# Performance work log

Measured on AMD Instinct MI355X. Metric: run time of the kernel, lower is better.

The kernel has to match this reference:

```python
import jax, jax.numpy as jnp
import numpy as np

N_NODES = 100000
N_EDGES = 1600000
D_IN = 128
D_OUT = 128


def setup_inputs() -> dict:
    key = jax.random.key(0)
    kx, ke, kw = jax.random.split(key, 3)
    x = jax.random.normal(kx, (N_NODES, D_IN), dtype=jnp.float32)
    edge_index = jax.random.randint(ke, (2, N_EDGES), 0, N_NODES, dtype=jnp.int32)
    W = jax.random.normal(kw, (D_IN, D_OUT), dtype=jnp.float32) / np.sqrt(D_IN)
    b = jnp.zeros((D_OUT,), dtype=jnp.float32)
    return {"x": x, "edge_index": edge_index, "W": W, "b": b}


def reference(x, edge_index, W, b):
    # PyG GCNConv: x' = D^{-1/2} (A + I) D^{-1/2} (x @ W) + b, then ReLU.
    n = x.shape[0]
    xw = x @ W  # linear transform first (as in GCNConv)
    # add self-loops
    loops = jnp.arange(n, dtype=edge_index.dtype)
    row = jnp.concatenate([edge_index[0], loops])  # source nodes
    col = jnp.concatenate([edge_index[1], loops])  # destination nodes
    # symmetric degree normalization (degree counted on destination, PyG-style)
    deg = jax.ops.segment_sum(jnp.ones_like(col, dtype=xw.dtype), col, num_segments=n)
    dinv = jnp.where(deg > 0, jax.lax.rsqrt(deg), 0.0)
    norm = dinv[row] * dinv[col]  # [E+N]
    # gather -> scale -> scatter-add
    msg = xw[row] * norm[:, None]  # [E+N, D_OUT]
    agg = jax.ops.segment_sum(msg, col, num_segments=n)  # [N, D_OUT]
    return jax.nn.relu(agg + b)
```

## Files before the change

kernel.cpp:

```cpp
#include <hip/hip_runtime.h>

#define DCH 128
#define T_PART 4096
#define B_MAX 512
#define CAPC 6144

typedef short bf16x8 __attribute__((ext_vector_type(8)));
typedef float f32x4 __attribute__((ext_vector_type(4)));

__device__ inline unsigned short f2bf(float f) {
    unsigned int u = __float_as_uint(f);
    unsigned int r = (u + 0x7fffu + ((u >> 16) & 1u)) >> 16;
    return (unsigned short)r;
}

__device__ inline void gload_lds16(const void* g, void* l) {
    __builtin_amdgcn_global_load_lds(
        (const __attribute__((address_space(1))) void*)g,
        (__attribute__((address_space(3))) void*)l, 16, 0, 0);
}

__global__ __launch_bounds__(256) void k_init(const float* __restrict__ W,
                                              unsigned short* __restrict__ Wf,
                                              int* __restrict__ gcount, int B) {
    int idx = blockIdx.x * 256 + threadIdx.x;
    if (idx < B) gcount[idx] = 0;
    int frag = blockIdx.x * 4 + (threadIdx.x >> 6);
    if (frag < 32) {
        int lane = threadIdx.x & 63;
        int nt = frag >> 2, ks = frag & 3;
        int nn = nt * 16 + (lane & 15);
        int k0 = ks * 32 + ((lane >> 4) * 8);
        unsigned short tmp[8];
#pragma unroll
        for (int j = 0; j < 8; ++j) tmp[j] = f2bf(W[(size_t)(k0 + j) * DCH + nn]);
        *(uint4*)&Wf[((size_t)frag * 64 + lane) * 8] = *(const uint4*)tmp;
    }
}

__global__ __launch_bounds__(512) void k_part(const int* __restrict__ row,
                                              const int* __restrict__ col,
                                              unsigned int* __restrict__ coarse,
                                              int* __restrict__ gcount,
                                              int E, int B) {
    __shared__ int hist[B_MAX];
    __shared__ int basex[B_MAX];
    __shared__ int curx[B_MAX];
    __shared__ int gb[B_MAX];
    __shared__ int wsum[8];
    __shared__ unsigned int spack[T_PART];
    __shared__ unsigned short sbuck[T_PART];

    int tid = threadIdx.x;
    int wv = tid >> 6, lane = tid & 63;
    int base_e = blockIdx.x * T_PART;
    int tileCnt = min(T_PART, E - base_e);

    hist[tid] = 0;
    __syncthreads();

    int er[8], ec[8];
#pragma unroll
    for (int i = 0; i < 8; ++i) {
        int e = base_e + tid + i * 512;
        if (e < E) {
            er[i] = row[e];
            ec[i] = col[e];
            atomicAdd(&hist[ec[i] >> 8], 1);
        } else {
            er[i] = -1;
            ec[i] = 0;
        }
    }
    __syncthreads();

    int v = hist[tid];
    int x = v;
#pragma unroll
    for (int o = 1; o < 64; o <<= 1) {
        int t = __shfl_up(x, o, 64);
        if (lane >= o) x += t;
    }
    if (lane == 63) wsum[wv] = x;
    __syncthreads();
    int add = 0;
    for (int w = 0; w < wv; ++w) add += wsum[w];
    int excl = x - v + add;
    basex[tid] = excl;
    curx[tid] = excl;
    if (tid < B) gb[tid] = (v > 0) ? atomicAdd(&gcount[tid], v) : 0;
    else gb[tid] = 0;
    __syncthreads();

#pragma unroll
    for (int i = 0; i < 8; ++i) {
        if (er[i] >= 0) {
            int b = ec[i] >> 8;
            int slot = atomicAdd(&curx[b], 1);
            spack[slot] = ((unsigned int)er[i] << 8) | (unsigned int)(ec[i] & 255);
            sbuck[slot] = (unsigned short)b;
        }
    }
    __syncthreads();

    for (int s = tid; s < tileCnt; s += 512) {
        int b = sbuck[s];
        int dst = gb[b] + (s - basex[b]);
        if (dst < CAPC) coarse[(size_t)b * CAPC + dst] = spack[s];
    }
}

__global__ __launch_bounds__(512) void k_csr(const unsigned int* __restrict__ coarse,
                                             const int* __restrict__ gcount,
                                             int* __restrict__ srow,
                                             int* __restrict__ off,
                                             int* __restrict__ cnt,
                                             int n, int B) {
    __shared__ unsigned int ent[CAPC];
    __shared__ int h[256], cur[256];
    __shared__ int red1[8], red2[4];
    __shared__ int bbase_s;

    int b = blockIdx.x;
    int tid = threadIdx.x;
    int wv = tid >> 6, lane = tid & 63;

    int part = 0;
    for (int i = tid; i < b; i += 512) part += gcount[i];
#pragma unroll
    for (int o = 1; o < 64; o <<= 1) part += __shfl_xor(part, o, 64);
    if (lane == 0) red1[wv] = part;
    if (tid < 256) h[tid] = 0;
    __syncthreads();
    if (tid == 0) {
        int s = 0;
        for (int w = 0; w < 8; ++w) s += red1[w];
        bbase_s = s;
    }
    int cntb = min(gcount[b], CAPC);
    for (int s = tid; s < cntb; s += 512) ent[s] = coarse[(size_t)b * CAPC + s];
    __syncthreads();

    for (int s = tid; s < cntb; s += 512) atomicAdd(&h[ent[s] & 255], 1);
    __syncthreads();

    int x = 0, v = 0;
    if (tid < 256) {
        v = h[tid];
        x = v;
#pragma unroll
        for (int o = 1; o < 64; o <<= 1) {
            int t = __shfl_up(x, o, 64);
            if (lane >= o) x += t;
        }
        if (lane == 63) red2[wv] = x;
    }
    __syncthreads();
    if (tid < 256) {
        int add = 0;
        for (int w = 0; w < wv; ++w) add += red2[w];
        int excl = x - v + add;
        cur[tid] = excl;
        int node = (b << 8) + tid;
        if (node < n) {
            cnt[node] = v;
            off[node] = bbase_s + excl;
        }
    }
    __syncthreads();

    int bbase = bbase_s;
    for (int s = tid; s < cntb; s += 512) {
        unsigned int p = ent[s];
        int d = p & 255;
        int slot = atomicAdd(&cur[d], 1);
        srow[bbase + slot] = (int)(p >> 8);
    }
}

__global__ __launch_bounds__(256) void k_gemm_mfma(const float* __restrict__ x,
                                                   const unsigned short* __restrict__ Wf,
                                                   const int* __restrict__ cnt,
                                                   unsigned short* __restrict__ y,
                                                   int n) {
    __shared__ char smem[64 * 512];
    int tid = threadIdx.x;
    int wv = tid >> 6;
    int lane = tid & 63;
    int blockRow = blockIdx.x * 64;

#pragma unroll
    for (int t = 0; t < 8; ++t) {
        int off = t * 4096 + wv * 1024 + lane * 16;
        int r = off >> 9;
        int gr = blockRow + r;
        if (gr >= n) gr = n - 1;
        int col = (off & 511) ^ ((r & 7) << 4);
        const char* src = (const char*)x + (size_t)gr * 512 + col;
        char* dst = smem + t * 4096 + wv * 1024;
        gload_lds16(src, dst);
    }
    __syncthreads();

    f32x4 acc[8];
    f32x4 zero = {0.f, 0.f, 0.f, 0.f};
#pragma unroll
    for (int t = 0; t < 8; ++t) acc[t] = zero;

    const bf16x8* wfv = (const bf16x8*)Wf;
    int rowL = wv * 16 + (lane & 15);
    int q = lane >> 4;
    int swz = (rowL & 7) << 4;
#pragma unroll
    for (int ks = 0; ks < 4; ++ks) {
        int colb = ks * 128 + q * 32;
        float4 lo = *(const float4*)&smem[(rowL * 512 + colb) ^ swz];
        float4 hi = *(const float4*)&smem[(rowL * 512 + colb + 16) ^ swz];
        bf16x8 a;
        a[0] = (short)f2bf(lo.x); a[1] = (short)f2bf(lo.y);
        a[2] = (short)f2bf(lo.z); a[3] = (short)f2bf(lo.w);
        a[4] = (short)f2bf(hi.x); a[5] = (short)f2bf(hi.y);
        a[6] = (short)f2bf(hi.z); a[7] = (short)f2bf(hi.w);
#pragma unroll
        for (int nt = 0; nt < 8; ++nt) {
            bf16x8 bfr = wfv[(nt * 4 + ks) * 64 + lane];
            acc[nt] = __builtin_amdgcn_mfma_f32_16x16x32_bf16(a, bfr, acc[nt], 0, 0, 0);
        }
    }

    int rowBase = blockRow + wv * 16;
    int orow_base = rowBase + q * 4;
#pragma unroll
    for (int r = 0; r < 4; ++r) {
        int orow = orow_base + r;
        if (orow < n) {
            float s = rsqrtf((float)(cnt[orow] + 1));
#pragma unroll
            for (int nt = 0; nt < 8; ++nt) {
                y[(size_t)orow * DCH + nt * 16 + (lane & 15)] = f2bf(acc[nt][r] * s);
            }
        }
    }
}

__global__ __launch_bounds__(256) void k_agg(const uint4* __restrict__ y4,
                                             const int* __restrict__ srow,
                                             const int* __restrict__ off,
                                             const float* __restrict__ b,
                                             float* __restrict__ out, int n, int E) {
    int i = blockIdx.x * 4 + (threadIdx.x >> 6);
    if (i >= n) return;
    int lane = threadIdx.x & 63;
    int q = lane >> 4;
    int l16 = lane & 15;
    int s = off[i];
    int e = (i + 1 < n) ? off[i + 1] : E;

    float acc[8];
#pragma unroll
    for (int k = 0; k < 8; ++k) acc[k] = 0.f;

    if (q == 0) {
        uint4 v = y4[(size_t)i * 16 + l16];
        unsigned int p[4] = {v.x, v.y, v.z, v.w};
#pragma unroll
        for (int t = 0; t < 4; ++t) {
            acc[2 * t]     += __uint_as_float(p[t] << 16);
            acc[2 * t + 1] += __uint_as_float(p[t] & 0xffff0000u);
        }
    }

    int j = s;
    for (; j + 16 <= e; j += 16) {
        int s0 = srow[j + q];
        int s1 = srow[j + 4 + q];
        int s2 = srow[j + 8 + q];
        int s3 = srow[j + 12 + q];
        uint4 v0 = y4[(size_t)s0 * 16 + l16];
        uint4 v1 = y4[(size_t)s1 * 16 + l16];
        uint4 v2 = y4[(size_t)s2 * 16 + l16];
        uint4 v3 = y4[(size_t)s3 * 16 + l16];
        unsigned int p0[4] = {v0.x, v0.y, v0.z, v0.w};
        unsigned int p1[4] = {v1.x, v1.y, v1.z, v1.w};
        unsigned int p2[4] = {v2.x, v2.y, v2.z, v2.w};
        unsigned int p3[4] = {v3.x, v3.y, v3.z, v3.w};
#pragma unroll
        for (int t = 0; t < 4; ++t) {
            acc[2 * t]     += __uint_as_float(p0[t] << 16);
            acc[2 * t + 1] += __uint_as_float(p0[t] & 0xffff0000u);
            acc[2 * t]     += __uint_as_float(p1[t] << 16);
            acc[2 * t + 1] += __uint_as_float(p1[t] & 0xffff0000u);
            acc[2 * t]     += __uint_as_float(p2[t] << 16);
            acc[2 * t + 1] += __uint_as_float(p2[t] & 0xffff0000u);
            acc[2 * t]     += __uint_as_float(p3[t] << 16);
            acc[2 * t + 1] += __uint_as_float(p3[t] & 0xffff0000u);
        }
    }
    for (; j + 8 <= e; j += 8) {
        int s0 = srow[j + q];
        int s1 = srow[j + 4 + q];
        uint4 v0 = y4[(size_t)s0 * 16 + l16];
        uint4 v1 = y4[(size_t)s1 * 16 + l16];
        unsigned int p0[4] = {v0.x, v0.y, v0.z, v0.w};
        unsigned int p1[4] = {v1.x, v1.y, v1.z, v1.w};
#pragma unroll
        for (int t = 0; t < 4; ++t) {
            acc[2 * t]     += __uint_as_float(p0[t] << 16);
            acc[2 * t + 1] += __uint_as_float(p0[t] & 0xffff0000u);
            acc[2 * t]     += __uint_as_float(p1[t] << 16);
            acc[2 * t + 1] += __uint_as_float(p1[t] & 0xffff0000u);
        }
    }
    for (; j + 4 <= e; j += 4) {
        int s0 = srow[j + q];
        uint4 v0 = y4[(size_t)s0 * 16 + l16];
        unsigned int p0[4] = {v0.x, v0.y, v0.z, v0.w};
#pragma unroll
        for (int t = 0; t < 4; ++t) {
            acc[2 * t]     += __uint_as_float(p0[t] << 16);
            acc[2 * t + 1] += __uint_as_float(p0[t] & 0xffff0000u);
        }
    }
    if (j + q < e) {
        int s0 = srow[j + q];
        uint4 v0 = y4[(size_t)s0 * 16 + l16];
        unsigned int p0[4] = {v0.x, v0.y, v0.z, v0.w};
#pragma unroll
        for (int t = 0; t < 4; ++t) {
            acc[2 * t]     += __uint_as_float(p0[t] << 16);
            acc[2 * t + 1] += __uint_as_float(p0[t] & 0xffff0000u);
        }
    }

#pragma unroll
    for (int k = 0; k < 8; ++k) {
        acc[k] += __shfl_xor(acc[k], 16, 64);
        acc[k] += __shfl_xor(acc[k], 32, 64);
    }

    if (q == 0) {
        float sc = rsqrtf((float)(e - s + 1));
        int c0 = l16 * 8;
        float4 b0 = *(const float4*)&b[c0];
        float4 b1 = *(const float4*)&b[c0 + 4];
        f32x4 o0, o1;
        o0[0] = fmaxf(fmaf(sc, acc[0], b0.x), 0.f);
        o0[1] = fmaxf(fmaf(sc, acc[1], b0.y), 0.f);
        o0[2] = fmaxf(fmaf(sc, acc[2], b0.z), 0.f);
        o0[3] = fmaxf(fmaf(sc, acc[3], b0.w), 0.f);
        o1[0] = fmaxf(fmaf(sc, acc[4], b1.x), 0.f);
        o1[1] = fmaxf(fmaf(sc, acc[5], b1.y), 0.f);
        o1[2] = fmaxf(fmaf(sc, acc[6], b1.z), 0.f);
        o1[3] = fmaxf(fmaf(sc, acc[7], b1.w), 0.f);
        f32x4* orow = (f32x4*)&out[(size_t)i * DCH + c0];
        __builtin_nontemporal_store(o0, &orow[0]);
        __builtin_nontemporal_store(o1, &orow[1]);
    }
}

extern "C" void kernel_launch(void* const* d_in, const int* in_sizes, int n_in,
                              void* d_out, int out_size, void* d_ws, size_t ws_size,
                              hipStream_t stream) {
    const float* x = (const float*)d_in[0];
    const int* ei  = (const int*)d_in[1];
    const float* W = (const float*)d_in[2];
    const float* b = (const float*)d_in[3];
    float* out = (float*)d_out;

    int n = in_sizes[0] / DCH;
    int E = in_sizes[1] / 2;
    const int* row = ei;
    const int* col = ei + E;

    int B = (n + 255) / 256;

    char* ws = (char*)d_ws;
    size_t o = 0;
    auto alloc = [&](size_t bytes) -> void* {
        o = (o + 255) & ~(size_t)255;
        void* p = ws + o;
        o += bytes;
        return p;
    };
    int* cnt     = (int*)alloc((size_t)n * 4);
    int* off     = (int*)alloc((size_t)(n + 1) * 4);
    int* gcount  = (int*)alloc((size_t)B * 4);
    int* srow    = (int*)alloc((size_t)E * 4);
    unsigned int* coarse = (unsigned int*)alloc((size_t)B * CAPC * 4);
    unsigned short* Wf = (unsigned short*)alloc((size_t)DCH * DCH * 2);
    unsigned short* y  = (unsigned short*)alloc((size_t)n * DCH * 2);

    int nt = (E + T_PART - 1) / T_PART;
    k_init<<<8, 256, 0, stream>>>(W, Wf, gcount, B);
    k_part<<<nt, 512, 0, stream>>>(row, col, coarse, gcount, E, B);
    k_csr<<<B, 512, 0, stream>>>(coarse, gcount, srow, off, cnt, n, B);
    k_gemm_mfma<<<(n + 63) / 64, 256, 0, stream>>>(x, Wf, cnt, y, n);
    k_agg<<<(n + 3) / 4, 256, 0, stream>>>((const uint4*)y, srow, off, b, out, n, E);
}
```

Measured before the change: 205.5 us.

## Fuse edge partitioning with GEMM in one launch; move source scaling to aggregation

Merges the edge-partition kernel and the x@W MFMA GEMM into one launch, with the block index picking the role, so the two independent stages can run concurrently. The GEMM no longer needs the degree counts, so the source-side D^{-1/2} scaling moves into the aggregation, which now loads a per-source dinv and uses FMAs. k_csr writes dinv directly. The aggregation gains an extra gather per edge, and the GEMM role now uses 128-row tiles over 512 threads in a 64KB shared buffer, which may lower occupancy.

```diff
diff --git a/kernel.cpp b/kernel.cpp
--- a/kernel.cpp
+++ b/kernel.cpp
@@ -38,75 +38,138 @@
     }
 }
 
-__global__ __launch_bounds__(512) void k_part(const int* __restrict__ row,
-                                              const int* __restrict__ col,
-                                              unsigned int* __restrict__ coarse,
-                                              int* __restrict__ gcount,
-                                              int E, int B) {
-    __shared__ int hist[B_MAX];
-    __shared__ int basex[B_MAX];
-    __shared__ int curx[B_MAX];
-    __shared__ int gb[B_MAX];
-    __shared__ int wsum[8];
-    __shared__ unsigned int spack[T_PART];
-    __shared__ unsigned short sbuck[T_PART];
+__global__ __launch_bounds__(512) void k_fused(const int* __restrict__ row,
+                                               const int* __restrict__ col,
+                                               unsigned int* __restrict__ coarse,
+                                               int* __restrict__ gcount,
+                                               const float* __restrict__ x,
+                                               const unsigned short* __restrict__ Wf,
+                                               unsigned short* __restrict__ y,
+                                               int E, int B, int nPart, int n) {
+    __shared__ uint4 smem4[4096];
+    char* smem = (char*)smem4;
 
     int tid = threadIdx.x;
     int wv = tid >> 6, lane = tid & 63;
-    int base_e = blockIdx.x * T_PART;
-    int tileCnt = min(T_PART, E - base_e);
-
-    hist[tid] = 0;
-    __syncthreads();
-
-    int er[8], ec[8];
-#pragma unroll
-    for (int i = 0; i < 8; ++i) {
-        int e = base_e + tid + i * 512;
-        if (e < E) {
-            er[i] = row[e];
-            ec[i] = col[e];
-            atomicAdd(&hist[ec[i] >> 8], 1);
-        } else {
-            er[i] = -1;
-            ec[i] = 0;
-        }
-    }
-    __syncthreads();
-
-    int v = hist[tid];
-    int x = v;
-#pragma unroll
-    for (int o = 1; o < 64; o <<= 1) {
-        int t = __shfl_up(x, o, 64);
-        if (lane >= o) x += t;
-    }
-    if (lane == 63) wsum[wv] = x;
-    __syncthreads();
-    int add = 0;
-    for (int w = 0; w < wv; ++w) add += wsum[w];
-    int excl = x - v + add;
-    basex[tid] = excl;
-    curx[tid] = excl;
-    if (tid < B) gb[tid] = (v > 0) ? atomicAdd(&gcount[tid], v) : 0;
-    else gb[tid] = 0;
-    __syncthreads();
-
-#pragma unroll
-    for (int i = 0; i < 8; ++i) {
-        if (er[i] >= 0) {
-            int b = ec[i] >> 8;
-            int slot = atomicAdd(&curx[b], 1);
-            spack[slot] = ((unsigned int)er[i] << 8) | (unsigned int)(ec[i] & 255);
-            sbuck[slot] = (unsigned short)b;
-        }
-    }
-    __syncthreads();
-
-    for (int s = tid; s < tileCnt; s += 512) {
-        int b = sbuck[s];
-        int dst = gb[b] + (s - basex[b]);
-        if (dst < CAPC) coarse[(size_t)b * CAPC + dst] = spack[s];
+
+    if (blockIdx.x < nPart) {
+        int* hist  = (int*)smem;
+        int* basex = (int*)(smem + 2048);
+        int* curx  = (int*)(smem + 4096);
+        int* gb    = (int*)(smem + 6144);
+        int* wsum  = (int*)(smem + 8192);
+        unsigned int*   spack = (unsigned int*)(smem + 8320);
+        unsigned short* sbuck = (unsigned short*)(smem + 24704);
+
+        int base_e = blockIdx.x * T_PART;
+        int tileCnt = min(T_PART, E - base_e);
+
+        hist[tid] = 0;
+        __syncthreads();
+
+        int er[8], ec[8];
+#pragma unroll
+        for (int i = 0; i < 8; ++i) {
+            int e = base_e + tid + i * 512;
+            if (e < E) {
+                er[i] = row[e];
+                ec[i] = col[e];
+                atomicAdd(&hist[ec[i] >> 8], 1);
+            } else {
+                er[i] = -1;
+                ec[i] = 0;
+            }
+        }
+        __syncthreads();
+
+        int v = hist[tid];
+        int x2 = v;
+#pragma unroll
+        for (int o = 1; o < 64; o <<= 1) {
+            int t = __shfl_up(x2, o, 64);
+            if (lane >= o) x2 += t;
+        }
+        if (lane == 63) wsum[wv] = x2;
+        __syncthreads();
+        int add = 0;
+        for (int w = 0; w < wv; ++w) add += wsum[w];
+        int excl = x2 - v + add;
+        basex[tid] = excl;
+        curx[tid] = excl;
+        if (tid < B) gb[tid] = (v > 0) ? atomicAdd(&gcount[tid], v) : 0;
+        else gb[tid] = 0;
+        __syncthreads();
+
+#pragma unroll
+        for (int i = 0; i < 8; ++i) {
+            if (er[i] >= 0) {
+                int bb = ec[i] >> 8;
+                int slot = atomicAdd(&curx[bb], 1);
+                spack[slot] = ((unsigned int)er[i] << 8) | (unsigned int)(ec[i] & 255);
+                sbuck[slot] = (unsigned short)bb;
+            }
+        }
+        __syncthreads();
+
+        for (int s = tid; s < tileCnt; s += 512) {
+            int bb = sbuck[s];
+            int dst = gb[bb] + (s - basex[bb]);
+            if (dst < CAPC) coarse[(size_t)bb * CAPC + dst] = spack[s];
+        }
+    } else {
+        int blockRow = (blockIdx.x - nPart) * 128;
+
+#pragma unroll
+        for (int t = 0; t < 8; ++t) {
+            int off = t * 8192 + wv * 1024 + lane * 16;
+            int r = off >> 9;
+            int gr = blockRow + r;
+            if (gr >= n) gr = n - 1;
+            int colb = (off & 511) ^ ((r & 7) << 4);
+            const char* src = (const char*)x + (size_t)gr * 512 + colb;
+            char* dst = smem + t * 8192 + wv * 1024;
+            gload_lds16(src, dst);
+        }
+        __syncthreads();
+
+        f32x4 acc[8];
+        f32x4 zero = {0.f, 0.f, 0.f, 0.f};
+#pragma unroll
+        for (int t = 0; t < 8; ++t) acc[t] = zero;
+
+        const bf16x8* wfv = (const bf16x8*)Wf;
+        int rowL = wv * 16 + (lane & 15);
+        int q = lane >> 4;
+        int swz = (rowL & 7) << 4;
+#pragma unroll
+        for (int ks = 0; ks < 4; ++ks) {
+            int colb = ks * 128 + q * 32;
+            float4 lo = *(const float4*)&smem[(rowL * 512 + colb) ^ swz];
+            float4 hi = *(const float4*)&smem[(rowL * 512 + colb + 16) ^ swz];
+            bf16x8 a;
+            a[0] = (short)f2bf(lo.x); a[1] = (short)f2bf(lo.y);
+            a[2] = (short)f2bf(lo.z); a[3] = (short)f2bf(lo.w);
+            a[4] = (short)f2bf(hi.x); a[5] = (short)f2bf(hi.y);
+            a[6] = (short)f2bf(hi.z); a[7] = (short)f2bf(hi.w);
+#pragma unroll
+            for (int nt = 0; nt < 8; ++nt) {
+                bf16x8 bfr = wfv[(nt * 4 + ks) * 64 + lane];
+                acc[nt] = __builtin_amdgcn_mfma_f32_16x16x32_bf16(a, bfr, acc[nt], 0, 0, 0);
+            }
+        }
+
+        int rowBase = blockRow + wv * 16;
+        int orow_base = rowBase + q * 4;
+#pragma unroll
+        for (int r = 0; r < 4; ++r) {
+            int orow = orow_base + r;
+            if (orow < n) {
+#pragma unroll
+                for (int nt = 0; nt < 8; ++nt) {
+                    y[(size_t)orow * DCH + nt * 16 + (lane & 15)] = f2bf(acc[nt][r]);
+                }
+            }
+        }
     }
 }
 
@@ -114,7 +177,7 @@
                                              const int* __restrict__ gcount,
                                              int* __restrict__ srow,
                                              int* __restrict__ off,
-                                             int* __restrict__ cnt,
+                                             float* __restrict__ dinvf,
                                              int n, int B) {
     __shared__ unsigned int ent[CAPC];
     __shared__ int h[256], cur[256];
@@ -163,8 +226,8 @@
         cur[tid] = excl;
         int node = (b << 8) + tid;
         if (node < n) {
-            cnt[node] = v;
             off[node] = bbase_s + excl;
+            dinvf[node] = rsqrtf((float)(v + 1));
         }
     }
     __syncthreads();
@@ -178,74 +241,10 @@
     }
 }
 
-__global__ __launch_bounds__(256) void k_gemm_mfma(const float* __restrict__ x,
-                                                   const unsigned short* __restrict__ Wf,
-                                                   const int* __restrict__ cnt,
-                                                   unsigned short* __restrict__ y,
-                                                   int n) {
-    __shared__ char smem[64 * 512];
-    int tid = threadIdx.x;
-    int wv = tid >> 6;
-    int lane = tid & 63;
-    int blockRow = blockIdx.x * 64;
-
-#pragma unroll
-    for (int t = 0; t < 8; ++t) {
-        int off = t * 4096 + wv * 1024 + lane * 16;
-        int r = off >> 9;
-        int gr = blockRow + r;
-        if (gr >= n) gr = n - 1;
-        int col = (off & 511) ^ ((r & 7) << 4);
-        const char* src = (const char*)x + (size_t)gr * 512 + col;
-        char* dst = smem + t * 4096 + wv * 1024;
-        gload_lds16(src, dst);
-    }
-    __syncthreads();
-
-    f32x4 acc[8];
-    f32x4 zero = {0.f, 0.f, 0.f, 0.f};
-#pragma unroll
-    for (int t = 0; t < 8; ++t) acc[t] = zero;
-
-    const bf16x8* wfv = (const bf16x8*)Wf;
-    int rowL = wv * 16 + (lane & 15);
-    int q = lane >> 4;
-    int swz = (rowL & 7) << 4;
-#pragma unroll
-    for (int ks = 0; ks < 4; ++ks) {
-        int colb = ks * 128 + q * 32;
-        float4 lo = *(const float4*)&smem[(rowL * 512 + colb) ^ swz];
-        float4 hi = *(const float4*)&smem[(rowL * 512 + colb + 16) ^ swz];
-        bf16x8 a;
-        a[0] = (short)f2bf(lo.x); a[1] = (short)f2bf(lo.y);
-        a[2] = (short)f2bf(lo.z); a[3] = (short)f2bf(lo.w);
-        a[4] = (short)f2bf(hi.x); a[5] = (short)f2bf(hi.y);
-        a[6] = (short)f2bf(hi.z); a[7] = (short)f2bf(hi.w);
-#pragma unroll
-        for (int nt = 0; nt < 8; ++nt) {
-            bf16x8 bfr = wfv[(nt * 4 + ks) * 64 + lane];
-            acc[nt] = __builtin_amdgcn_mfma_f32_16x16x32_bf16(a, bfr, acc[nt], 0, 0, 0);
-        }
-    }
-
-    int rowBase = blockRow + wv * 16;
-    int orow_base = rowBase + q * 4;
-#pragma unroll
-    for (int r = 0; r < 4; ++r) {
-        int orow = orow_base + r;
-        if (orow < n) {
-            float s = rsqrtf((float)(cnt[orow] + 1));
-#pragma unroll
-            for (int nt = 0; nt < 8; ++nt) {
-                y[(size_t)orow * DCH + nt * 16 + (lane & 15)] = f2bf(acc[nt][r] * s);
-            }
-        }
-    }
-}
-
 __global__ __launch_bounds__(256) void k_agg(const uint4* __restrict__ y4,
                                              const int* __restrict__ srow,
                                              const int* __restrict__ off,
+                                             const float* __restrict__ dinv,
                                              const float* __restrict__ b,
                                              float* __restrict__ out, int n, int E) {
     int i = blockIdx.x * 4 + (threadIdx.x >> 6);
@@ -255,6 +254,7 @@
     int l16 = lane & 15;
     int s = off[i];
     int e = (i + 1 < n) ? off[i + 1] : E;
+    float di = dinv[i];
 
     float acc[8];
 #pragma unroll
@@ -265,8 +265,8 @@
         unsigned int p[4] = {v.x, v.y, v.z, v.w};
 #pragma unroll
         for (int t = 0; t < 4; ++t) {
-            acc[2 * t]     += __uint_as_float(p[t] << 16);
-            acc[2 * t + 1] += __uint_as_float(p[t] & 0xffff0000u);
+            acc[2 * t]     = fmaf(di, __uint_as_float(p[t] << 16), acc[2 * t]);
+            acc[2 * t + 1] = fmaf(di, __uint_as_float(p[t] & 0xffff0000u), acc[2 * t + 1]);
         }
     }
 
@@ -276,6 +276,7 @@
         int s1 = srow[j + 4 + q];
         int s2 = srow[j + 8 + q];
         int s3 = srow[j + 12 + q];
+        float d0 = dinv[s0], d1 = dinv[s1], d2 = dinv[s2], d3 = dinv[s3];
         uint4 v0 = y4[(size_t)s0 * 16 + l16];
         uint4 v1 = y4[(size_t)s1 * 16 + l16];
         uint4 v2 = y4[(size_t)s2 * 16 + l16];
@@ -286,49 +287,52 @@
         unsigned int p3[4] = {v3.x, v3.y, v3.z, v3.w};
 #pragma unroll
         for (int t = 0; t < 4; ++t) {
-            acc[2 * t]     += __uint_as_float(p0[t] << 16);
-            acc[2 * t + 1] += __uint_as_float(p0[t] & 0xffff0000u);
-            acc[2 * t]     += __uint_as_float(p1[t] << 16);
-            acc[2 * t + 1] += __uint_as_float(p1[t] & 0xffff0000u);
-            acc[2 * t]     += __uint_as_float(p2[t] << 16);
-            acc[2 * t + 1] += __uint_as_float(p2[t] & 0xffff0000u);
-            acc[2 * t]     += __uint_as_float(p3[t] << 16);
-            acc[2 * t + 1] += __uint_as_float(p3[t] & 0xffff0000u);
+            acc[2 * t]     = fmaf(d0, __uint_as_float(p0[t] << 16), acc[2 * t]);
+            acc[2 * t + 1] = fmaf(d0, __uint_as_float(p0[t] & 0xffff0000u), acc[2 * t + 1]);
+            acc[2 * t]     = fmaf(d1, __uint_as_float(p1[t] << 16), acc[2 * t]);
+            acc[2 * t + 1] = fmaf(d1, __uint_as_float(p1[t] & 0xffff0000u), acc[2 * t + 1]);
+            acc[2 * t]     = fmaf(d2, __uint_as_float(p2[t] << 16), acc[2 * t]);
+            acc[2 * t + 1] = fmaf(d2, __uint_as_float(p2[t] & 0xffff0000u), acc[2 * t + 1]);
+            acc[2 * t]     = fmaf(d3, __uint_as_float(p3[t] << 16), acc[2 * t]);
+            acc[2 * t + 1] = fmaf(d3, __uint_as_float(p3[t] & 0xffff0000u), acc[2 * t + 1]);
         }
     }
     for (; j + 8 <= e; j += 8) {
         int s0 = srow[j + q];
         int s1 = srow[j + 4 + q];
+        float d0 = dinv[s0], d1 = dinv[s1];
         uint4 v0 = y4[(size_t)s0 * 16 + l16];
         uint4 v1 = y4[(size_t)s1 * 16 + l16];
         unsigned int p0[4] = {v0.x, v0.y, v0.z, v0.w};
         unsigned int p1[4] = {v1.x, v1.y, v1.z, v1.w};
 #pragma unroll
         for (int t = 0; t < 4; ++t) {
-            acc[2 * t]     += __uint_as_float(p0[t] << 16);
-            acc[2 * t + 1] += __uint_as_float(p0[t] & 0xffff0000u);
-            acc[2 * t]     += __uint_as_float(p1[t] << 16);
-            acc[2 * t + 1] += __uint_as_float(p1[t] & 0xffff0000u);
+            acc[2 * t]     = fmaf(d0, __uint_as_float(p0[t] << 16), acc[2 * t]);
+            acc[2 * t + 1] = fmaf(d0, __uint_as_float(p0[t] & 0xffff0000u), acc[2 * t + 1]);
+            acc[2 * t]     = fmaf(d1, __uint_as_float(p1[t] << 16), acc[2 * t]);
+            acc[2 * t + 1] = fmaf(d1, __uint_as_float(p1[t] & 0xffff0000u), acc[2 * t + 1]);
         }
     }
     for (; j + 4 <= e; j += 4) {
         int s0 = srow[j + q];
+        float d0 = dinv[s0];
         uint4 v0 = y4[(size_t)s0 * 16 + l16];
         unsigned int p0[4] = {v0.x, v0.y, v0.z, v0.w};
 #pragma unroll
         for (int t = 0; t < 4; ++t) {
-            acc[2 * t]     += __uint_as_float(p0[t] << 16);
-            acc[2 * t + 1] += __uint_as_float(p0[t] & 0xffff0000u);
+            acc[2 * t]     = fmaf(d0, __uint_as_float(p0[t] << 16), acc[2 * t]);
+            acc[2 * t + 1] = fmaf(d0, __uint_as_float(p0[t] & 0xffff0000u), acc[2 * t + 1]);
         }
     }
     if (j + q < e) {
         int s0 = srow[j + q];
+        float d0 = dinv[s0];
         uint4 v0 = y4[(size_t)s0 * 16 + l16];
         unsigned int p0[4] = {v0.x, v0.y, v0.z, v0.w};
 #pragma unroll
         for (int t = 0; t < 4; ++t) {
-            acc[2 * t]     += __uint_as_float(p0[t] << 16);
-            acc[2 * t + 1] += __uint_as_float(p0[t] & 0xffff0000u);
+            acc[2 * t]     = fmaf(d0, __uint_as_float(p0[t] << 16), acc[2 * t]);
+            acc[2 * t + 1] = fmaf(d0, __uint_as_float(p0[t] & 0xffff0000u), acc[2 * t + 1]);
         }
     }
 
@@ -339,7 +343,7 @@
     }
 
     if (q == 0) {
-        float sc = rsqrtf((float)(e - s + 1));
+        float sc = di;
         int c0 = l16 * 8;
         float4 b0 = *(const float4*)&b[c0];
         float4 b1 = *(const float4*)&b[c0 + 4];
@@ -382,7 +386,7 @@
         o += bytes;
         return p;
     };
-    int* cnt     = (int*)alloc((size_t)n * 4);
+    float* dinvf = (float*)alloc((size_t)n * 4);
     int* off     = (int*)alloc((size_t)(n + 1) * 4);
     int* gcount  = (int*)alloc((size_t)B * 4);
     int* srow    = (int*)alloc((size_t)E * 4);
@@ -391,9 +395,11 @@
     unsigned short* y  = (unsigned short*)alloc((size_t)n * DCH * 2);
 
     int nt = (E + T_PART - 1) / T_PART;
+    int gemmBlocks = (n + 127) / 128;
     k_init<<<8, 256, 0, stream>>>(W, Wf, gcount, B);
-    k_part<<<nt, 512, 0, stream>>>(row, col, coarse, gcount, E, B);
-    k_csr<<<B, 512, 0, stream>>>(coarse, gcount, srow, off, cnt, n, B);
-    k_gemm_mfma<<<(n + 63) / 64, 256, 0, stream>>>(x, Wf, cnt, y, n);
-    k_agg<<<(n + 3) / 4, 256, 0, stream>>>((const uint4*)y, srow, off, b, out, n, E);
-}
+    k_fused<<<nt + gemmBlocks, 512, 0, stream>>>(row, col, coarse, gcount,
+                                                 x, Wf, y, E, B, nt, n);
+    k_csr<<<B, 512, 0, stream>>>(coarse, gcount, srow, off, dinvf, n, B);
+    k_agg<<<(n + 3) / 4, 256, 0, stream>>>((const uint4*)y, srow, off, dinvf,
+                                           b, out, n, E);
+}
```

After: 202.3 us. No clear change (-1.6%).
